# Kernel optimization log

Measured on AMD Instinct MI355X. Metric: run time of the kernel, lower is better.

## Reference

```python
import jax, jax.numpy as jnp
import numpy as np

N_SAMPLES = 2 ** 15            # 32768
N_FRAMES = N_SAMPLES // 256    # 128 (window 512, step 256)
N_EVENTS = 8
N_HARM = 8
TOTAL_COEFFS = N_SAMPLES // 2 + 1
NOISE_SPEC = 16
NYQUIST = 22050.0 / 2.0
MAX_F = 3000.0 / NYQUIST
MIN_F = 20.0 / NYQUIST
F_SPAN = MAX_F - MIN_F
Y = 20 + NOISE_SPEC + N_FRAMES + N_HARM   # 172
DIM = Y + 128 + 128                        # 428
BATCH = 16


def lin_interp(x, out_size):
    # torch F.interpolate(mode='linear', align_corners=False) along last dim
    n = x.shape[-1]
    scale = n / out_size
    coords = jnp.clip((jnp.arange(out_size) + 0.5) * scale - 0.5, 0.0, n - 1.0)
    lo = jnp.floor(coords).astype(jnp.int32)
    hi = jnp.minimum(lo + 1, n - 1)
    w = (coords - lo).astype(x.dtype)
    return x[..., lo] * (1.0 - w) + x[..., hi] * w


def setup_inputs() -> dict:
    key = jax.random.key(0)
    k1, k2 = jax.random.split(key)
    x = jax.random.normal(k1, (BATCH, N_EVENTS, DIM), dtype=jnp.float32)
    noise = jax.random.uniform(k2, (BATCH, N_EVENTS, N_SAMPLES), dtype=jnp.float32)
    return {"x": x, "noise": noise}


def reference(x, noise):
    B = x.shape[0]
    x = jax.nn.sigmoid(x)
    means = x[..., 0:1]
    stds = x[..., 1:2] * 0.1
    amps = x[..., 2:3] ** 2
    f0 = x[..., 3:4] ** 2
    factors = 1.0 + x[..., 4:12] * 7.0
    mags = (x[..., 12:20] * 0.9999) ** 2
    noise_coeff = x[..., 20:20 + NOISE_SPEC]
    fine_env = x[..., 36:36 + N_FRAMES] * 2.0 - 1.0
    amp_factors = x[..., 164:172] ** 2
    f0_var = x[..., 172:300]

    # fine amplitude envelope: cumsum over frames, clamp, upsample
    fe = jnp.clip(jnp.cumsum(fine_env.reshape(-1, N_FRAMES), axis=-1), 0.0, 1.0)
    fe = lin_interp(fe, N_SAMPLES).reshape(B, N_EVENTS, N_SAMPLES)

    # localized band-limited noise, gaussian time window
    rng = jnp.arange(N_SAMPLES, dtype=x.dtype)
    mu = jnp.clip(means * N_SAMPLES, -(N_SAMPLES // 2), N_SAMPLES * 1.5)
    sigma = jnp.clip((1e-8 + stds) * N_SAMPLES, 0.0, N_SAMPLES - 1.0)
    z = (rng - mu) / sigma                                   # (B,E,S)
    probs = jnp.exp(-0.5 * z * z) / (sigma * np.sqrt(2.0 * np.pi))
    probs = probs / (jnp.max(jnp.abs(probs), axis=-1, keepdims=True) + 1e-12)
    u = noise * 2.0 - 1.0                                    # uniform(-1,1)
    spec_shape = lin_interp(noise_coeff, TOTAL_COEFFS)       # (B,E,total_coeffs)
    ns = jnp.fft.rfft(u, axis=-1, norm='ortho') * spec_shape
    nz = jnp.fft.irfft(ns, n=N_SAMPLES, axis=-1, norm='ortho')
    atoms = probs * nz * amps * fe                           # (B,E,S)

    # harmonic resonance
    f0f = f0.reshape(-1, 1)                                  # (BE,1)
    var = f0_var.reshape(-1, N_FRAMES) * (f0f * 0.01)        # (BE,F)
    f0t = lin_interp(f0f + var, N_SAMPLES)                   # (BE,S)
    f0t = MIN_F + f0t * F_SPAN
    f0t = jnp.where(f0t > 1.0, 0.0, f0t)
    fac = factors.reshape(-1, N_HARM).at[:, 0].set(1.0)      # (BE,H)
    freqs = f0t[:, None, :] * fac[:, :, None] * np.pi        # (BE,H,S)
    osc = jnp.sin(jnp.cumsum(freqs, axis=-1)) * amp_factors.reshape(-1, N_HARM, 1)
    # cumprod of a constant per frame == geometric powers
    mg = mags.reshape(-1, N_HARM, 1) ** jnp.arange(1, N_FRAMES + 1, dtype=x.dtype)
    mg = lin_interp(mg, N_SAMPLES)                           # (BE,H,S)
    res = jnp.sum(osc * mg, axis=1).reshape(B, N_EVENTS, N_SAMPLES)

    # fft convolution (zero-padded to 2S to avoid circular wrap)
    pa = jnp.pad(atoms, ((0, 0), (0, 0), (0, N_SAMPLES)))
    pr = jnp.pad(res, ((0, 0), (0, 0), (0, N_SAMPLES)))
    conv = jnp.fft.irfft(jnp.fft.rfft(pa, axis=-1) * jnp.fft.rfft(pr, axis=-1),
                         n=2 * N_SAMPLES, axis=-1)[..., :N_SAMPLES]
    return jnp.sum(conv, axis=1, keepdims=True)              # (B,1,S)
```

## Files before the change

### kernel.cpp

```cpp
#include <hip/hip_runtime.h>
#include <math.h>

#define NSAMP 32768
#define NFFT2 65536
#define NFRM 128
#define PSTRIDE 2688
#define P_FEPAIR 64
#define P_PW2 320
#define P_LQ 1344
#define P_AF 1604
#define P_END 2636
#define TWO_PI_F 6.28318530717958647692f

typedef float2 cplx;

__device__ __forceinline__ cplx cmul_(cplx a, cplx b){ return make_float2(a.x*b.x - a.y*b.y, a.x*b.y + a.y*b.x); }
__device__ __forceinline__ cplx cadd_(cplx a, cplx b){ return make_float2(a.x+b.x, a.y+b.y); }
__device__ __forceinline__ cplx csub_(cplx a, cplx b){ return make_float2(a.x-b.x, a.y-b.y); }

template<bool INV>
__device__ __forceinline__ void dft4_(cplx x0,cplx x1,cplx x2,cplx x3, cplx&y0,cplx&y1,cplx&y2,cplx&y3){
  cplx t0=cadd_(x0,x2), t1=csub_(x0,x2), t2=cadd_(x1,x3), t3=csub_(x1,x3);
  y0=cadd_(t0,t2); y2=csub_(t0,t2);
  cplx it3 = make_float2(-t3.y, t3.x);
  if (INV){ y1=cadd_(t1,it3); y3=csub_(t1,it3); }
  else    { y1=csub_(t1,it3); y3=cadd_(t1,it3); }
}

template<bool INV>
__device__ __forceinline__ void dft8ip_(cplx* v){
  cplx e0,e1,e2,e3,o0,o1,o2,o3;
  dft4_<INV>(v[0],v[2],v[4],v[6], e0,e1,e2,e3);
  dft4_<INV>(v[1],v[3],v[5],v[7], o0,o1,o2,o3);
  const float r = 0.70710678118654752440f;
  cplx w1 = INV ? make_float2(r, r)    : make_float2(r,-r);
  cplx w2 = INV ? make_float2(0.f,1.f) : make_float2(0.f,-1.f);
  cplx w3 = INV ? make_float2(-r,r)    : make_float2(-r,-r);
  cplx t1 = cmul_(o1,w1), t2 = cmul_(o2,w2), t3 = cmul_(o3,w3);
  v[0]=cadd_(e0,o0); v[4]=csub_(e0,o0);
  v[1]=cadd_(e1,t1); v[5]=csub_(e1,t1);
  v[2]=cadd_(e2,t2); v[6]=csub_(e2,t2);
  v[3]=cadd_(e3,t3); v[7]=csub_(e3,t3);
}

template<bool INV>
__device__ __forceinline__ void dft16ip_(cplx* v){
  cplx t0[4], t1[4], t2[4], t3[4];
  dft4_<INV>(v[0], v[4], v[8],  v[12], t0[0],t0[1],t0[2],t0[3]);
  dft4_<INV>(v[1], v[5], v[9],  v[13], t1[0],t1[1],t1[2],t1[3]);
  dft4_<INV>(v[2], v[6], v[10], v[14], t2[0],t2[1],t2[2],t2[3]);
  dft4_<INV>(v[3], v[7], v[11], v[15], t3[0],t3[1],t3[2],t3[3]);
  const float C1=0.92387953251128675613f, S1=0.38268343236508977172f, R2=0.70710678118654752440f;
  #define TWD_(x, cc, ss) (INV ? cmul_((x), make_float2((cc), (ss))) : cmul_((x), make_float2((cc), -(ss))))
  t1[1] = TWD_(t1[1], C1, S1);
  t1[2] = TWD_(t1[2], R2, R2);
  t1[3] = TWD_(t1[3], S1, C1);
  t2[1] = TWD_(t2[1], R2, R2);
  t2[2] = TWD_(t2[2], 0.f, 1.f);
  t2[3] = TWD_(t2[3], -R2, R2);
  t3[1] = TWD_(t3[1], S1, C1);
  t3[2] = TWD_(t3[2], -R2, R2);
  t3[3] = TWD_(t3[3], -C1, -S1);
  #undef TWD_
  dft4_<INV>(t0[0], t1[0], t2[0], t3[0], v[0], v[4], v[8],  v[12]);
  dft4_<INV>(t0[1], t1[1], t2[1], t3[1], v[1], v[5], v[9],  v[13]);
  dft4_<INV>(t0[2], t1[2], t2[2], t3[2], v[2], v[6], v[10], v[14]);
  dft4_<INV>(t0[3], t1[3], t2[3], t3[3], v[3], v[7], v[11], v[15]);
}

template<int R0, bool INV>
__device__ __forceinline__ void fft_core(float* lre, float* lim, int t){
  constexpr int Q = R0/16;
  constexpr int S1 = R0 + 8;
  int g = t >> 4, a = t & 15;
  cplx v[Q];
  #pragma unroll
  for (int bb=0;bb<Q;bb++){ int idx = g*S1 + a + 16*bb; v[bb]=make_float2(lre[idx],lim[idx]); }
  if constexpr (Q==16) dft16ip_<INV>(v); else dft8ip_<INV>(v);
  float th = (INV?TWO_PI_F:-TWO_PI_F)*(float)a/(float)R0;
  float sn,cs; __sincosf(th,&sn,&cs);
  cplx w1=make_float2(cs,sn), wu=w1;
  #pragma unroll
  for (int c=1;c<Q;c++){ v[c]=cmul_(v[c],wu); wu=cmul_(wu,w1); }
  __syncthreads();
  #pragma unroll
  for (int c=0;c<Q;c++){ int m = a*Q + ((c+a)&(Q-1)); lre[g*S1+m]=v[c].x; lim[g*S1+m]=v[c].y; }
  __syncthreads();
}

template<int R0, bool INV>
__device__ __forceinline__ bool fft_stage2(const float* lre, const float* lim, int t, int& g2, int& c2, cplx* z){
  constexpr int Q = R0/16; constexpr int S1 = R0+8;
  bool active = (R0==256) || (t < 16*Q);
  g2 = (R0==256)?(t>>4):(t>>3);
  c2 = (R0==256)?(t&15):(t&7);
  if (active){
    #pragma unroll
    for (int a2=0;a2<16;a2++){ int m = a2*Q + ((c2+a2)&(Q-1)); z[a2]=make_float2(lre[g2*S1+m], lim[g2*S1+m]); }
    dft16ip_<INV>(z);
  }
  return active;
}

__global__ __launch_bounds__(256) void k_fft_pack_fwd1(const float* __restrict__ noise, cplx* __restrict__ dst, float interBase){
  constexpr int Q=16, S1=264;
  __shared__ float lre[4352], lim[4352];
  int t=threadIdx.x;
  int bx=blockIdx.x;
  int sig = bx>>3;
  int tBase=(bx&7)*16;
  const float* n0 = noise + (size_t)(2*sig)*NSAMP;
  const float* n1 = noise + (size_t)(2*sig+1)*NSAMP;
  #pragma unroll
  for (int i=0;i<16;i++){
    int e=t+256*i, g=e&15, r=e>>4;
    int ts = tBase+g+128*r;
    lre[g*S1+r]=n0[ts]*2.f-1.f;
    lim[g*S1+r]=n1[ts]*2.f-1.f;
  }
  __syncthreads();
  fft_core<256,false>(lre,lim,t);
  int g2,c2; cplx z[16];
  fft_stage2<256,false>(lre,lim,t,g2,c2,z);
  int p=tBase+g2;
  float thp=interBase*(float)p;
  float snc,csc; __sincosf(thp*(float)c2,&snc,&csc);
  float sns,css; __sincosf(thp*(float)Q,&sns,&css);
  cplx wu=make_float2(csc,snc), ws=make_float2(css,sns);
  cplx* db = dst + (size_t)sig*NSAMP;
  size_t ob=(size_t)256*(size_t)p+(size_t)c2;
  #pragma unroll
  for (int d=0;d<16;d++){ db[ob+(size_t)(d*16)]=cmul_(z[d],wu); wu=cmul_(wu,ws); }
}

__device__ __forceinline__ void fft128_natural(float* re, float* im, int t){
  __syncthreads();
  fft_core<128,false>(re,im,t);
  int g2,c2; cplx z[16];
  bool act = fft_stage2<128,false>(re,im,t,g2,c2,z);
  __syncthreads();
  if (act){
    #pragma unroll
    for (int d=0;d<16;d++){ int u=c2+8*d; re[u*17+g2]=z[d].x; im[u*17+g2]=z[d].y; }
  }
  __syncthreads();
}

__global__ __launch_bounds__(256) void k_nfilter_ip1(const cplx* __restrict__ src, cplx* __restrict__ dst,
    const float* __restrict__ P){
  __shared__ float aRe[2176], aIm[2176], bRe[2176], bIm[2176];
  __shared__ float fRe[2176], fIm[2176];
  __shared__ float c1s[16], c2sh[16];
  int t=threadIdx.x, pb=blockIdx.x, j=blockIdx.y;
  const cplx* sb = src + ((size_t)j<<15);
  cplx* db = dst + ((size_t)j<<15);
  if (t<16) c1s[t] = P[(size_t)(2*j)*PSTRIDE+28+t];
  else if (t<32) c2sh[t-16] = P[(size_t)(2*j+1)*PSTRIDE+28+(t-16)];
  #pragma unroll
  for (int i=0;i<8;i++){
    int e=t+256*i, g=e&15, r=e>>4;
    int col = (pb<8)? (pb*16+g) : (g*16);
    cplx v = sb[col + (r<<8)];
    aRe[g*136+r]=v.x; aIm[g*136+r]=v.y;
  }
  fft128_natural(aRe,aIm,t);
  if (pb<8){
    #pragma unroll
    for (int i=0;i<8;i++){
      int e=t+256*i, g=e&15, r=e>>4;
      int col = 240-pb*16+g;
      cplx v = sb[col + (r<<8)];
      bRe[g*136+r]=v.x; bIm[g*136+r]=v.y;
    }
    fft128_natural(bRe,bIm,t);
  }
  const float inv32768 = 1.0f/32768.0f;
  if (pb<8){
    for (int s=0;s<2;s++){
      __syncthreads();
      #pragma unroll
      for (int uu=0; uu<8; uu++){
        int g=t&15, u=(t>>4)+16*uu;
        if (g!=0){
          int colK = s? (240-pb*16+g) : (pb*16+g);
          int gm=16-g, um=127-u;
          float Zkx,Zky,Zmx,Zmy;
          if (s==0){ Zkx=aRe[u*17+g]; Zky=aIm[u*17+g]; Zmx=bRe[um*17+gm]; Zmy=bIm[um*17+gm]; }
          else     { Zkx=bRe[u*17+g]; Zky=bIm[u*17+g]; Zmx=aRe[um*17+gm]; Zmy=aIm[um*17+gm]; }
          int k = colK + (u<<8);
          int kb = min(k, NSAMP-k);
          float coords=fminf(fmaxf((kb+0.5f)*(16.0f/16385.0f)-0.5f,0.0f),15.0f);
          int lo=(int)coords; float w=coords-lo; int hi=min(lo+1,15);
          float s1=(c1s[lo]+w*(c1s[hi]-c1s[lo]))*inv32768;
          float s2=(c2sh[lo]+w*(c2sh[hi]-c2sh[lo]))*inv32768;
          float U1x=0.5f*(Zkx+Zmx), U1y=0.5f*(Zky-Zmy);
          float U2x=0.5f*(Zky+Zmy), U2y=-0.5f*(Zkx-Zmx);
          fRe[g*136+u]=U1x*s1 - U2y*s2; fIm[g*136+u]=U1y*s1 + U2x*s2;
        }
      }
      __syncthreads();
      fft_core<128,true>(fRe,fIm,t);
      int gg,cc; cplx z[16];
      bool act = fft_stage2<128,true>(fRe,fIm,t,gg,cc,z);
      if (act && gg!=0){
        int p = (s==0) ? (pb*16+gg) : (240-pb*16+gg);
        float thp=(TWO_PI_F/32768.0f)*(float)p;
        float snc,csc; __sincosf(thp*(float)cc,&snc,&csc);
        float sns,css; __sincosf(thp*8.0f,&sns,&css);
        cplx wu=make_float2(csc,snc), wsx=make_float2(css,sns);
        int ob=128*p+cc;
        #pragma unroll
        for (int d=0;d<16;d++){ db[ob+8*d]=cmul_(z[d],wu); wu=cmul_(wu,wsx); }
      }
    }
  } else {
    __syncthreads();
    #pragma unroll
    for (int uu=0; uu<8; uu++){
      int g=t&15, u=(t>>4)+16*uu;
      int k = g*16 + (u<<8);
      int gm=(16-g)&15;
      int um=(g==0)? ((128-u)&127) : (127-u);
      float Zkx=aRe[u*17+g], Zky=aIm[u*17+g];
      float Zmx=aRe[um*17+gm], Zmy=aIm[um*17+gm];
      int kb = min(k, NSAMP-k);
      float coords=fminf(fmaxf((kb+0.5f)*(16.0f/16385.0f)-0.5f,0.0f),15.0f);
      int lo=(int)coords; float w=coords-lo; int hi=min(lo+1,15);
      float s1=(c1s[lo]+w*(c1s[hi]-c1s[lo]))*inv32768;
      float s2=(c2sh[lo]+w*(c2sh[hi]-c2sh[lo]))*inv32768;
      float U1x=0.5f*(Zkx+Zmx), U1y=0.5f*(Zky-Zmy);
      float U2x=0.5f*(Zky+Zmy), U2y=-0.5f*(Zkx-Zmx);
      fRe[g*136+u]=U1x*s1 - U2y*s2; fIm[g*136+u]=U1y*s1 + U2x*s2;
    }
    __syncthreads();
    fft_core<128,true>(fRe,fIm,t);
    int gg,cc; cplx z[16];
    bool act = fft_stage2<128,true>(fRe,fIm,t,gg,cc,z);
    if (act){
      int p = 16*gg;
      float thp=(TWO_PI_F/32768.0f)*(float)p;
      float snc,csc; __sincosf(thp*(float)cc,&snc,&csc);
      float sns,css; __sincosf(thp*8.0f,&sns,&css);
      cplx wu=make_float2(csc,snc), wsx=make_float2(css,sns);
      int ob=128*p+cc;
      #pragma unroll
      for (int d=0;d<16;d++){ db[ob+8*d]=cmul_(z[d],wu); wu=cmul_(wu,wsx); }
    }
  }
}

__global__ __launch_bounds__(256) void k_ifinal_split(const cplx* __restrict__ src, float* __restrict__ dstf){
  constexpr int S1=264;
  __shared__ float lre[4352], lim[4352];
  int t=threadIdx.x; int bx=blockIdx.x;
  int sig=bx>>3; int tBase=(bx&7)*16;
  const cplx* sb = src + (size_t)sig*NSAMP;
  #pragma unroll
  for (int i=0;i<16;i++){
    int e=t+256*i, g=e&15, r=e>>4;
    cplx vv = sb[tBase+g + (size_t)r*128];
    lre[g*S1+r]=vv.x; lim[g*S1+r]=vv.y;
  }
  __syncthreads();
  fft_core<256,true>(lre,lim,t);
  int g2,c2; cplx z[16];
  fft_stage2<256,true>(lre,lim,t,g2,c2,z);
  __syncthreads();
  #pragma unroll
  for (int d=0;d<16;d++){ int u=c2+16*d; lre[u*17+g2]=z[d].x; lim[u*17+g2]=z[d].y; }
  __syncthreads();
  float* p0 = dstf + (size_t)(2*sig)*NSAMP;
  float* p1 = dstf + (size_t)(2*sig+1)*NSAMP;
  #pragma unroll
  for (int i=0;i<16;i++){
    int e=t+256*i, g3=e&15, u=e>>4;
    int ts = tBase+g3+u*128;
    p0[ts]=lre[u*17+g3]; p1[ts]=lim[u*17+g3];
  }
}

__global__ __launch_bounds__(256) void k_conv_build_fwd1(const float* __restrict__ P,
    const float* __restrict__ NZf, cplx* __restrict__ dst, int rowBase, float interBase){
  constexpr int Q=16, S1=264;
  __shared__ float smem[8448];
  float* lre = smem;
  float* lim = smem + 4224;
  float* sTab = smem;
  int t=threadIdx.x;
  int row = rowBase + blockIdx.y;
  int tBase = blockIdx.x*16;
  const float* Pr = P + (size_t)row*PSTRIDE;
  for (int i=t; i<P_END; i+=256) sTab[i] = Pr[i];
  __syncthreads();
  float mu=sTab[0], sigma=sTab[1], amp=sTab[2], pscale=sTab[3];
  float fac[8], mh[8];
  #pragma unroll
  for (int h=0;h<8;h++){ fac[h]=sTab[4+h]; mh[h]=sTab[12+h]; }
  const float2* fe2 = (const float2*)&sTab[P_FEPAIR];
  const float*  pw2 = &sTab[P_PW2];
  const float2* LQt = (const float2*)&sTab[P_LQ];
  const float*  Af  = &sTab[P_AF];
  const float* nzrow = NZf + (size_t)row*NSAMP;
  float vre[8], vim[8];
  #pragma unroll
  for (int i=0;i<8;i++){
    int e=t+256*i, g=e&15, r=e>>4;
    int ts = tBase + g + (r<<8);
    float cc=fminf(fmaxf((ts+0.5f)*(1.0f/256.0f)-0.5f,0.0f),127.0f);
    int lo=(int)cc; float w=cc-lo;
    float2 fp = fe2[lo];
    float fev = fp.x + w*fp.y;
    int slot, n0;
    if (ts<128){ slot=0; n0=ts+1; } else { int km=(ts-128)>>8; slot=km+1; n0=ts-127-(km<<8); }
    float nf=(float)n0, nf2=nf*nf;
    float2 lq = LQt[slot];
    float base = nf*lq.x + nf2*lq.y;
    float wm = (lo<127)? w : 0.0f;
    float resv=0.f;
    #pragma unroll
    for (int h=0;h<8;h++){
      float mgb = pw2[h*128+lo];
      if (mgb > 1e-7f){
        float rr = Af[slot*8+h] + fac[h]*base;
        float fr = rr - floorf(rr);
        float s = __builtin_amdgcn_sinf(fr);
        resv += s*mgb*(1.0f + wm*(mh[h]-1.0f));
      }
    }
    float zz=((float)ts-mu)/sigma;
    float prb=pscale*__expf(-0.5f*zz*zz);
    vre[i] = prb*nzrow[ts]*amp*fev;
    vim[i] = resv;
  }
  __syncthreads();
  #pragma unroll
  for (int i=0;i<8;i++){
    int e=t+256*i, g=e&15, r=e>>4;
    lre[g*S1+r]=vre[i]; lim[g*S1+r]=vim[i];
  }
  #pragma unroll
  for (int i=8;i<16;i++){
    int e=t+256*i, g=e&15, r=e>>4;
    lre[g*S1+r]=0.f; lim[g*S1+r]=0.f;
  }
  __syncthreads();
  fft_core<256,false>(lre,lim,t);
  int g2,c2; cplx z[16];
  fft_stage2<256,false>(lre,lim,t,g2,c2,z);
  int p = tBase+g2;
  float thp = interBase*(float)p;
  float snc,csc; __sincosf(thp*(float)c2,&snc,&csc);
  float sns,css; __sincosf(thp*(float)Q,&sns,&css);
  cplx wu=make_float2(csc,snc), ws=make_float2(css,sns);
  cplx* db = dst + (size_t)blockIdx.y*NFFT2;
  size_t ob=(size_t)256*(size_t)p+(size_t)c2;
  #pragma unroll
  for (int d=0; d<16; d++){ db[ob+(size_t)(d*16)]=cmul_(z[d],wu); wu=cmul_(wu,ws); }
}

__global__ __launch_bounds__(256) void k_fwd2_sq(const cplx* __restrict__ C,
    cplx* __restrict__ D0, cplx* __restrict__ D1){
  constexpr int S1=264;
  __shared__ float lre[4352], lim[4352];
  int t=threadIdx.x;
  int tBase = blockIdx.x*16;
  int bLoc = blockIdx.y;
  int half = blockIdx.z;
  cplx* Dh = half ? D1 : D0;
  float accx[16], accy[16];
  #pragma unroll
  for (int d=0;d<16;d++){ accx[d]=0.f; accy[d]=0.f; }
  int g2=t>>4, c2=t&15;
  for (int e=0;e<4;e++){
    int sigLoc = bLoc*8 + half*4 + e;
    const cplx* sb = C + (size_t)sigLoc*NFFT2;
    __syncthreads();
    #pragma unroll
    for (int i=0;i<16;i++){
      int ee=t+256*i, g=ee&15, r=ee>>4;
      cplx vv = sb[tBase+g + (size_t)r*256];
      lre[g*S1+r]=vv.x; lim[g*S1+r]=vv.y;
    }
    __syncthreads();
    fft_core<256,false>(lre,lim,t);
    int gg,cc; cplx z[16];
    fft_stage2<256,false>(lre,lim,t,gg,cc,z);
    #pragma unroll
    for (int d=0;d<16;d++){
      float x=z[d].x, y=z[d].y;
      accx[d] += x*x - y*y;
      accy[d] += 2.f*x*y;
    }
  }
  __syncthreads();
  const float s = 1.0f/131072.0f;
  #pragma unroll
  for (int d=0;d<16;d++){ int u=c2+16*d; lre[u*17+g2]=accx[d]*s; lim[u*17+g2]=accy[d]*s; }
  __syncthreads();
  cplx* db = Dh + (size_t)bLoc*NFFT2;
  #pragma unroll
  for (int i=0;i<16;i++){
    int ee=t+256*i, g3=ee&15, u=ee>>4;
    db[tBase+g3 + (size_t)u*256] = make_float2(lre[u*17+g3], lim[u*17+g3]);
  }
}

__global__ __launch_bounds__(256) void k_inv1_sum(const cplx* __restrict__ D0, const cplx* __restrict__ D1,
    cplx* __restrict__ E){
  constexpr int Q=16, S1=264;
  __shared__ float lre[4352], lim[4352];
  int t=threadIdx.x, bx=blockIdx.x;
  int sig=bx>>4, tBase=(bx&15)*16;
  const cplx* s0 = D0 + (size_t)sig*NFFT2;
  const cplx* s1 = D1 + (size_t)sig*NFFT2;
  cplx* db = E + (size_t)sig*NFFT2;
  #pragma unroll
  for (int i=0;i<16;i++){
    int e=t+256*i, g=e&15, r=e>>4;
    size_t idx = tBase+g + (size_t)r*256;
    cplx a=s0[idx], b=s1[idx];
    lre[g*S1+r]=a.x+b.x; lim[g*S1+r]=a.y+b.y;
  }
  __syncthreads();
  fft_core<256,true>(lre,lim,t);
  int g2,c2; cplx z[16];
  fft_stage2<256,true>(lre,lim,t,g2,c2,z);
  int p = tBase+g2;
  float thp = (TWO_PI_F/65536.0f)*(float)p;
  float snc,csc; __sincosf(thp*(float)c2,&snc,&csc);
  float sns,css; __sincosf(thp*(float)Q,&sns,&css);
  cplx wu=make_float2(csc,snc), ws=make_float2(css,sns);
  size_t ob=(size_t)256*(size_t)p+(size_t)c2;
  #pragma unroll
  for (int d=0; d<16; d++){ db[ob+(size_t)(d*16)]=cmul_(z[d],wu); wu=cmul_(wu,ws); }
}

__global__ __launch_bounds__(256) void k_final_imout(const cplx* __restrict__ E, float* __restrict__ out,
    int batchBase){
  constexpr int S1=264;
  __shared__ float lre[4352], lim[4352];
  int t=threadIdx.x; int bx=blockIdx.x;
  int sig=bx>>4; int tBase=(bx&15)*16;
  const cplx* sb = E + (size_t)sig*NFFT2;
  #pragma unroll
  for (int i=0;i<16;i++){
    int e=t+256*i, g=e&15, r=e>>4;
    cplx vv = sb[tBase+g+(size_t)r*256];
    lre[g*S1+r]=vv.x; lim[g*S1+r]=vv.y;
  }
  __syncthreads();
  fft_core<256,true>(lre,lim,t);
  int g2,c2; cplx z[16];
  fft_stage2<256,true>(lre,lim,t,g2,c2,z);
  __syncthreads();
  #pragma unroll
  for (int d=0;d<16;d++){ int u=c2+16*d; lre[u*17+g2]=z[d].y; }
  __syncthreads();
  float* o = out + (size_t)(batchBase+sig)*NSAMP;
  #pragma unroll
  for (int i=0;i<8;i++){
    int e=t+256*i, g3=e&15, u=e>>4;
    o[tBase+g3 + u*256] = lre[u*17+g3];
  }
}

__global__ __launch_bounds__(256) void k_params(const float* __restrict__ x, float* __restrict__ P){
  int row = blockIdx.x; int t = threadIdx.x;
  const float* xr = x + row*428;
  float* Pr = P + (size_t)row*PSTRIDE;
  __shared__ float sx[428];
  __shared__ float fes[128], f0s[128];
  __shared__ double Cds[128];
  __shared__ float facs[8], ms[8], afs[8];
  __shared__ float f0_sh;
  for (int i=t;i<428;i+=256) sx[i]=1.0f/(1.0f+expf(-xr[i]));
  __syncthreads();
  if (t==0){
    float mean = sx[0]; float stds = sx[1]*0.1f; float amp = sx[2]*sx[2];
    float mu = fminf(fmaxf(mean*32768.0f, -16384.0f), 49152.0f);
    float sigma = fminf(fmaxf((1e-8f + stds)*32768.0f, 0.0f), 32767.0f);
    float c = 1.0f/(sigma*2.5066282746310002f);
    float tt0 = fminf(fmaxf(floorf(mu), 0.0f), 32767.0f);
    float tt1 = fminf(fmaxf(ceilf(mu), 0.0f), 32767.0f);
    float z0 = (tt0-mu)/sigma, z1=(tt1-mu)/sigma;
    float gmax = fmaxf(expf(-0.5f*z0*z0), expf(-0.5f*z1*z1));
    float pscale = c / (c*gmax + 1e-12f);
    Pr[0]=mu; Pr[1]=sigma; Pr[2]=amp; Pr[3]=pscale;
  }
  if (t<8){
    float fv = (t==0)?1.0f:(1.0f+sx[4+t]*7.0f);
    facs[t]=fv; Pr[4+t]=fv;
    float m = sx[12+t]*0.9999f; m=m*m; ms[t]=m; Pr[12+t]=m;
    afs[t]=sx[164+t]*sx[164+t];
  }
  if (t>=32&&t<48) Pr[28+(t-32)] = sx[20+(t-32)];
  if (t==64) f0_sh = sx[3]*sx[3];
  if (t==65){
    float acc=0.f;
    for (int f=0;f<128;f++){ acc += sx[36+f]*2.0f-1.0f; fes[f]=fminf(fmaxf(acc,0.f),1.f); }
  }
  __syncthreads();
  if (t<128){
    float f0=f0_sh;
    f0s[t] = f0 + sx[172+t]*(f0*0.01f);
  }
  __syncthreads();
  if (t==0){
    double acc = 128.0*(double)f0s[0]; Cds[0]=acc;
    for (int k=0;k<127;k++){ acc += 128.0*((double)f0s[k]+(double)f0s[k+1]); Cds[k+1]=acc; }
  }
  if (t<128){
    float v=fes[t], vh=fes[min(t+1,127)];
    Pr[P_FEPAIR+2*t]=v; Pr[P_FEPAIR+2*t+1]=vh-v;
  }
  if (t>=128 && t<136){
    int h=t-128; float m=ms[h];
    float acc = afs[h]*m;
    float* dstp = Pr + P_PW2 + h*128;
    dstp[0]=acc;
    for (int f=1;f<128;f++){ acc*=m; dstp[f]=acc; }
  }
  __syncthreads();
  const double MINF_D=20.0/11025.0, FSPAN_D=2980.0/11025.0;
  if (t<129){
    int k=t-1;
    float Lb, Qb;
    if (k<0){ Lb=(float)(0.5*(MINF_D+FSPAN_D*(double)f0s[0])); Qb=0.f; }
    else {
      double f0k=(double)f0s[k];
      double d=(k<127)?((double)f0s[k+1]-f0k):0.0;
      Lb=(float)(0.5*(MINF_D+FSPAN_D*f0k));
      Qb=(float)(0.5*FSPAN_D*d*(1.0/512.0));
    }
    Pr[P_LQ+2*t]=Lb; Pr[P_LQ+2*t+1]=Qb;
  }
  for (int idx=t; idx<129*8; idx+=256){
    int jj=idx>>3, h=idx&7, k=jj-1;
    float Aval;
    if (k<0) Aval=0.f;
    else {
      double phi0=(double)(128+256*k)*MINF_D+FSPAN_D*Cds[k];
      Aval=(float)(0.5*fmod((double)facs[h]*phi0,2.0));
    }
    Pr[P_AF+idx]=Aval;
  }
}

extern "C" void kernel_launch(void* const* d_in, const int* in_sizes, int n_in,
                              void* d_out, int out_size, void* d_ws, size_t ws_size,
                              hipStream_t stream){
  const float* x = (const float*)d_in[0];
  const float* noise = (const float*)d_in[1];
  float* out = (float*)d_out;
  char* ws = (char*)d_ws;

  const size_t szN = (size_t)64*NSAMP*sizeof(cplx);
  const size_t szD = (size_t)16*NFFT2*sizeof(cplx);
  const size_t oA = (size_t)2<<20;
  const size_t oB = oA + szN;
  const size_t oD0 = oB + szN;
  const size_t oD1 = oD0 + szD;
  const size_t oE  = oD1 + szD;
  const size_t oC  = oE + szD;

  const int cand[5] = {1,2,4,8,16};
  int nchunk = -1;
  for (int ci=0; ci<5; ci++){
    size_t csz = ((size_t)(128/cand[ci]))*NFFT2*sizeof(cplx);
    if (oC + csz <= ws_size){ nchunk = cand[ci]; break; }
  }
  if (nchunk < 0) return;
  int sigPerChunk = 128/nchunk;
  int bpc = sigPerChunk/8;

  float* P = (float*)(ws);
  cplx* A = (cplx*)(ws + oA);
  cplx* B = (cplx*)(ws + oB);
  cplx* D0 = (cplx*)(ws + oD0);
  cplx* D1 = (cplx*)(ws + oD1);
  cplx* E  = (cplx*)(ws + oE);
  cplx* C  = (cplx*)(ws + oC);

  k_params<<<128, 256, 0, stream>>>(x, P);
  k_fft_pack_fwd1<<<512, 256, 0, stream>>>(noise, A, -TWO_PI_F/32768.0f);
  k_nfilter_ip1<<<dim3(9,64), 256, 0, stream>>>(A, B, P);
  k_ifinal_split<<<512, 256, 0, stream>>>(B, (float*)A);

  for (int c=0; c<nchunk; c++){
    int rowBase = c*sigPerChunk;
    int batchBase = c*bpc;
    k_conv_build_fwd1<<<dim3(16, sigPerChunk), 256, 0, stream>>>(P, (float*)A, C, rowBase, -TWO_PI_F/65536.0f);
    k_fwd2_sq<<<dim3(16, bpc, 2), 256, 0, stream>>>(C, D0, D1);
    k_inv1_sum<<<bpc*16, 256, 0, stream>>>(D0, D1, E);
    k_final_imout<<<bpc*16, 256, 0, stream>>>(E, out, batchBase);
  }
}
```

Before: 130.4 us.

## Store intermediate spectra as packed bf16 and fuse squaring with first inverse FFT pass

The first-pass FFT output of the conv build stage is now stored as packed bf16 real/imag pairs in one 32-bit word, which halves the traffic for the largest intermediate buffer. The squaring/accumulation kernel now runs the first inverse FFT pass in place and writes two partial halves. The final kernel sums those halves, exploiting the linearity of the FFT. This removes one kernel launch and a full round trip of the D buffers through global memory. In exchange, precision drops to bf16 on the intermediate spectrum, and the inverse pass is done twice (once per half).

```diff
diff --git a/kernel.cpp b/kernel.cpp
--- a/kernel.cpp
+++ b/kernel.cpp
@@ -17,6 +17,14 @@
 __device__ __forceinline__ cplx cmul_(cplx a, cplx b){ return make_float2(a.x*b.x - a.y*b.y, a.x*b.y + a.y*b.x); }
 __device__ __forceinline__ cplx cadd_(cplx a, cplx b){ return make_float2(a.x+b.x, a.y+b.y); }
 __device__ __forceinline__ cplx csub_(cplx a, cplx b){ return make_float2(a.x-b.x, a.y-b.y); }
+
+__device__ __forceinline__ unsigned int packbf2(float re, float im){
+  unsigned int ur = __float_as_uint(re);
+  unsigned int ui = __float_as_uint(im);
+  ur = (ur + 0x7FFFu + ((ur>>16)&1u)) >> 16;
+  ui = (ui + 0x7FFFu + ((ui>>16)&1u)) & 0xFFFF0000u;
+  return ur | ui;
+}
 
 template<bool INV>
 __device__ __forceinline__ void dft4_(cplx x0,cplx x1,cplx x2,cplx x3, cplx&y0,cplx&y1,cplx&y2,cplx&y3){
@@ -280,7 +288,7 @@
 }
 
 __global__ __launch_bounds__(256) void k_conv_build_fwd1(const float* __restrict__ P,
-    const float* __restrict__ NZf, cplx* __restrict__ dst, int rowBase, float interBase){
+    const float* __restrict__ NZf, unsigned int* __restrict__ dst, int rowBase, float interBase){
   constexpr int Q=16, S1=264;
   __shared__ float smem[8448];
   float* lre = smem;
@@ -352,34 +360,39 @@
   float snc,csc; __sincosf(thp*(float)c2,&snc,&csc);
   float sns,css; __sincosf(thp*(float)Q,&sns,&css);
   cplx wu=make_float2(csc,snc), ws=make_float2(css,sns);
-  cplx* db = dst + (size_t)blockIdx.y*NFFT2;
+  unsigned int* db = dst + (size_t)blockIdx.y*NFFT2;
   size_t ob=(size_t)256*(size_t)p+(size_t)c2;
   #pragma unroll
-  for (int d=0; d<16; d++){ db[ob+(size_t)(d*16)]=cmul_(z[d],wu); wu=cmul_(wu,ws); }
-}
-
-__global__ __launch_bounds__(256) void k_fwd2_sq(const cplx* __restrict__ C,
-    cplx* __restrict__ D0, cplx* __restrict__ D1){
-  constexpr int S1=264;
+  for (int d=0; d<16; d++){
+    cplx val = cmul_(z[d],wu);
+    db[ob+(size_t)(d*16)] = packbf2(val.x, val.y);
+    wu=cmul_(wu,ws);
+  }
+}
+
+__global__ __launch_bounds__(256) void k_sq_inv1(const unsigned int* __restrict__ C,
+    cplx* __restrict__ E0, cplx* __restrict__ E1){
+  constexpr int Q=16, S1=264;
   __shared__ float lre[4352], lim[4352];
   int t=threadIdx.x;
   int tBase = blockIdx.x*16;
   int bLoc = blockIdx.y;
   int half = blockIdx.z;
-  cplx* Dh = half ? D1 : D0;
+  cplx* Eh = half ? E1 : E0;
   float accx[16], accy[16];
   #pragma unroll
   for (int d=0;d<16;d++){ accx[d]=0.f; accy[d]=0.f; }
   int g2=t>>4, c2=t&15;
   for (int e=0;e<4;e++){
     int sigLoc = bLoc*8 + half*4 + e;
-    const cplx* sb = C + (size_t)sigLoc*NFFT2;
+    const unsigned int* sb = C + (size_t)sigLoc*NFFT2;
     __syncthreads();
     #pragma unroll
     for (int i=0;i<16;i++){
       int ee=t+256*i, g=ee&15, r=ee>>4;
-      cplx vv = sb[tBase+g + (size_t)r*256];
-      lre[g*S1+r]=vv.x; lim[g*S1+r]=vv.y;
+      unsigned int u = sb[tBase+g + (size_t)r*256];
+      lre[g*S1+r]=__uint_as_float(u<<16);
+      lim[g*S1+r]=__uint_as_float(u & 0xFFFF0000u);
     }
     __syncthreads();
     fft_core<256,false>(lre,lim,t);
@@ -395,58 +408,40 @@
   __syncthreads();
   const float s = 1.0f/131072.0f;
   #pragma unroll
-  for (int d=0;d<16;d++){ int u=c2+16*d; lre[u*17+g2]=accx[d]*s; lim[u*17+g2]=accy[d]*s; }
-  __syncthreads();
-  cplx* db = Dh + (size_t)bLoc*NFFT2;
-  #pragma unroll
-  for (int i=0;i<16;i++){
-    int ee=t+256*i, g3=ee&15, u=ee>>4;
-    db[tBase+g3 + (size_t)u*256] = make_float2(lre[u*17+g3], lim[u*17+g3]);
-  }
-}
-
-__global__ __launch_bounds__(256) void k_inv1_sum(const cplx* __restrict__ D0, const cplx* __restrict__ D1,
-    cplx* __restrict__ E){
-  constexpr int Q=16, S1=264;
-  __shared__ float lre[4352], lim[4352];
-  int t=threadIdx.x, bx=blockIdx.x;
-  int sig=bx>>4, tBase=(bx&15)*16;
-  const cplx* s0 = D0 + (size_t)sig*NFFT2;
-  const cplx* s1 = D1 + (size_t)sig*NFFT2;
-  cplx* db = E + (size_t)sig*NFFT2;
-  #pragma unroll
-  for (int i=0;i<16;i++){
-    int e=t+256*i, g=e&15, r=e>>4;
-    size_t idx = tBase+g + (size_t)r*256;
-    cplx a=s0[idx], b=s1[idx];
-    lre[g*S1+r]=a.x+b.x; lim[g*S1+r]=a.y+b.y;
+  for (int d=0;d<16;d++){
+    int rrow = c2 + 16*d;
+    lre[g2*S1+rrow] = accx[d]*s;
+    lim[g2*S1+rrow] = accy[d]*s;
   }
   __syncthreads();
   fft_core<256,true>(lre,lim,t);
-  int g2,c2; cplx z[16];
-  fft_stage2<256,true>(lre,lim,t,g2,c2,z);
-  int p = tBase+g2;
+  int gg,cc; cplx z[16];
+  fft_stage2<256,true>(lre,lim,t,gg,cc,z);
+  int p = tBase+gg;
   float thp = (TWO_PI_F/65536.0f)*(float)p;
-  float snc,csc; __sincosf(thp*(float)c2,&snc,&csc);
+  float snc,csc; __sincosf(thp*(float)cc,&snc,&csc);
   float sns,css; __sincosf(thp*(float)Q,&sns,&css);
   cplx wu=make_float2(csc,snc), ws=make_float2(css,sns);
-  size_t ob=(size_t)256*(size_t)p+(size_t)c2;
+  cplx* db = Eh + (size_t)bLoc*NFFT2;
+  size_t ob=(size_t)256*(size_t)p+(size_t)cc;
   #pragma unroll
   for (int d=0; d<16; d++){ db[ob+(size_t)(d*16)]=cmul_(z[d],wu); wu=cmul_(wu,ws); }
 }
 
-__global__ __launch_bounds__(256) void k_final_imout(const cplx* __restrict__ E, float* __restrict__ out,
-    int batchBase){
+__global__ __launch_bounds__(256) void k_final_imout(const cplx* __restrict__ E0, const cplx* __restrict__ E1,
+    float* __restrict__ out, int batchBase){
   constexpr int S1=264;
   __shared__ float lre[4352], lim[4352];
   int t=threadIdx.x; int bx=blockIdx.x;
   int sig=bx>>4; int tBase=(bx&15)*16;
-  const cplx* sb = E + (size_t)sig*NFFT2;
+  const cplx* s0 = E0 + (size_t)sig*NFFT2;
+  const cplx* s1 = E1 + (size_t)sig*NFFT2;
   #pragma unroll
   for (int i=0;i<16;i++){
     int e=t+256*i, g=e&15, r=e>>4;
-    cplx vv = sb[tBase+g+(size_t)r*256];
-    lre[g*S1+r]=vv.x; lim[g*S1+r]=vv.y;
+    size_t idx = tBase+g+(size_t)r*256;
+    cplx a=s0[idx], b=s1[idx];
+    lre[g*S1+r]=a.x+b.x; lim[g*S1+r]=a.y+b.y;
   }
   __syncthreads();
   fft_core<256,true>(lre,lim,t);
@@ -555,18 +550,17 @@
   char* ws = (char*)d_ws;
 
   const size_t szN = (size_t)64*NSAMP*sizeof(cplx);
-  const size_t szD = (size_t)16*NFFT2*sizeof(cplx);
-  const size_t oA = (size_t)2<<20;
-  const size_t oB = oA + szN;
-  const size_t oD0 = oB + szN;
-  const size_t oD1 = oD0 + szD;
-  const size_t oE  = oD1 + szD;
-  const size_t oC  = oE + szD;
+  const size_t szE = (size_t)16*NFFT2*sizeof(cplx);
+  const size_t oA  = (size_t)2<<20;
+  const size_t oB  = oA + szN;
+  const size_t oE0 = oB + szN;
+  const size_t oE1 = oE0 + szE;
+  const size_t oC  = oE1 + szE;
 
   const int cand[5] = {1,2,4,8,16};
   int nchunk = -1;
   for (int ci=0; ci<5; ci++){
-    size_t csz = ((size_t)(128/cand[ci]))*NFFT2*sizeof(cplx);
+    size_t csz = ((size_t)(128/cand[ci]))*NFFT2*sizeof(unsigned int);
     if (oC + csz <= ws_size){ nchunk = cand[ci]; break; }
   }
   if (nchunk < 0) return;
@@ -576,10 +570,9 @@
   float* P = (float*)(ws);
   cplx* A = (cplx*)(ws + oA);
   cplx* B = (cplx*)(ws + oB);
-  cplx* D0 = (cplx*)(ws + oD0);
-  cplx* D1 = (cplx*)(ws + oD1);
-  cplx* E  = (cplx*)(ws + oE);
-  cplx* C  = (cplx*)(ws + oC);
+  cplx* E0 = (cplx*)(ws + oE0);
+  cplx* E1 = (cplx*)(ws + oE1);
+  unsigned int* C = (unsigned int*)(ws + oC);
 
   k_params<<<128, 256, 0, stream>>>(x, P);
   k_fft_pack_fwd1<<<512, 256, 0, stream>>>(noise, A, -TWO_PI_F/32768.0f);
@@ -590,8 +583,7 @@
     int rowBase = c*sigPerChunk;
     int batchBase = c*bpc;
     k_conv_build_fwd1<<<dim3(16, sigPerChunk), 256, 0, stream>>>(P, (float*)A, C, rowBase, -TWO_PI_F/65536.0f);
-    k_fwd2_sq<<<dim3(16, bpc, 2), 256, 0, stream>>>(C, D0, D1);
-    k_inv1_sum<<<bpc*16, 256, 0, stream>>>(D0, D1, E);
-    k_final_imout<<<bpc*16, 256, 0, stream>>>(E, out, batchBase);
-  }
-}
+    k_sq_inv1<<<dim3(16, bpc, 2), 256, 0, stream>>>(C, E0, E1);
+    k_final_imout<<<bpc*16, 256, 0, stream>>>(E0, E1, out, batchBase);
+  }
+}
```

After: 116.1 us. 10.9% less time.
